# Performance work log

Hardware: AMD Instinct MI355X
Metric: run time of the kernel (lower is better)

## Reference

```python
import jax, jax.numpy as jnp
import numpy as np

D_MODEL = 512
NUM_HEADS = 8
HEAD_DIM = D_MODEL // NUM_HEADS  # 64


def setup_inputs() -> dict:
    key = jax.random.key(0)
    k_x, k_wqkv, k_bqkv, k_wout, k_bout = jax.random.split(key, 5)
    B, L = 30, 2048
    s_in = 1.0 / np.sqrt(D_MODEL)
    return {
        "x": jax.random.normal(k_x, (B, L, D_MODEL), dtype=jnp.float32),
        "w_qkv": jax.random.uniform(k_wqkv, (3 * D_MODEL, D_MODEL), minval=-s_in, maxval=s_in, dtype=jnp.float32),
        "b_qkv": jax.random.uniform(k_bqkv, (3 * D_MODEL,), minval=-s_in, maxval=s_in, dtype=jnp.float32),
        "w_out": jax.random.uniform(k_wout, (D_MODEL, D_MODEL), minval=-s_in, maxval=s_in, dtype=jnp.float32),
        "b_out": jax.random.uniform(k_bout, (D_MODEL,), minval=-s_in, maxval=s_in, dtype=jnp.float32),
    }


def reference(x, w_qkv, b_qkv, w_out, b_out):
    B, L, _ = x.shape
    # QKV projection: (B, L, 3*d_model)
    qkv = jnp.einsum("bld,ed->ble", x, w_qkv) + b_qkv
    # NOTE: source discards the permute, so layout stays (B, L, H, 3*head_dim)
    qkv = qkv.reshape(B, L, NUM_HEADS, 3 * HEAD_DIM)
    q, k, v = jnp.split(qkv, 3, axis=-1)  # each (B, L, H, head_dim)
    # Attention contracts head_dim -> (B, L, H, H): attention OVER HEADS, faithful to bug
    scores = jnp.einsum("blhd,blgd->blhg", q, k) / np.sqrt(HEAD_DIM)
    # mask=False in source adds 0 -> no-op
    attn = jax.nn.softmax(scores, axis=-1)
    val = jnp.einsum("blhg,blgd->blhd", attn, v).reshape(B, L, D_MODEL)
    out = jnp.einsum("bld,ed->ble", val, w_out) + b_out
    return out
```

## Files before the change

### kernel.cpp

```cpp
#include <hip/hip_runtime.h>
#include <hip/hip_bf16.h>
#include <stdint.h>

typedef short    s16x8  __attribute__((ext_vector_type(8)));
typedef __bf16   bf16x8 __attribute__((ext_vector_type(8)));
typedef float    f32x4  __attribute__((ext_vector_type(4)));

__device__ __forceinline__ unsigned short f2bf(float f) {
    union { float f; unsigned u; } v; v.f = f;
    unsigned r = v.u + 0x7FFFu + ((v.u >> 16) & 1u);
    return (unsigned short)(r >> 16);
}
__device__ __forceinline__ float bf2f(unsigned short s) {
    union { unsigned u; float f; } v; v.u = ((unsigned)s) << 16;
    return v.f;
}

__device__ __forceinline__ void gload16(const void* g, void* l) {
    __builtin_amdgcn_global_load_lds(
        (const __attribute__((address_space(1))) void*)(uintptr_t)g,
        (__attribute__((address_space(3))) void*)(uintptr_t)l,
        16, 0, 0);
}

__global__ __launch_bounds__(256) void cvt_bf16(const float* __restrict__ in,
                                                unsigned short* __restrict__ out,
                                                int n4) {
    int i = blockIdx.x * blockDim.x + threadIdx.x;
    int stride = gridDim.x * blockDim.x;
    for (; i < n4; i += stride) {
        const float4 v = *(const float4*)(in + (size_t)i * 4);
        ushort4 o;
        o.x = f2bf(v.x); o.y = f2bf(v.y); o.z = f2bf(v.z); o.w = f2bf(v.w);
        *(ushort4*)(out + (size_t)i * 4) = o;
    }
}

template<bool OUT_BF16>
__global__ __launch_bounds__(256) void gemm_bt(
        const unsigned short* __restrict__ A,
        const unsigned short* __restrict__ B,
        const float* __restrict__ bias,
        void* __restrict__ Cvoid,
        int M, int N, int K) {
    constexpr int BM = 128, BN = 128, BK = 32;
    __shared__ unsigned short As[BM * BK];
    __shared__ unsigned short Bs[BN * BK];
    const int tid  = threadIdx.x;
    const int lane = tid & 63;
    const int wv   = tid >> 6;
    const int ntn  = N / BN;
    const int bm   = (int)blockIdx.x / ntn;
    const int bn   = (int)blockIdx.x % ntn;
    const int wr   = (wv >> 1) * 64;
    const int wc   = (wv & 1) * 64;
    const int lr   = lane & 15;
    const int lk   = (lane >> 4) * 8;

    f32x4 acc[4][4] = {};

    for (int k0 = 0; k0 < K; k0 += BK) {
        #pragma unroll
        for (int i = 0; i < 2; ++i) {
            int f   = i * 4096 + tid * 16;
            int row = f >> 6;
            int col = (f & 63) >> 1;
            gload16(A + (size_t)(bm * BM + row) * K + k0 + col, (char*)As + f);
            gload16(B + (size_t)(bn * BN + row) * K + k0 + col, (char*)Bs + f);
        }
        __syncthreads();

        bf16x8 af[4], bfr[4];
        #pragma unroll
        for (int m = 0; m < 4; ++m)
            af[m] = *(const bf16x8*)(As + (wr + m * 16 + lr) * BK + lk);
        #pragma unroll
        for (int n = 0; n < 4; ++n)
            bfr[n] = *(const bf16x8*)(Bs + (wc + n * 16 + lr) * BK + lk);
        #pragma unroll
        for (int m = 0; m < 4; ++m)
            #pragma unroll
            for (int n = 0; n < 4; ++n)
                acc[m][n] = __builtin_amdgcn_mfma_f32_16x16x32_bf16(
                    af[m], bfr[n], acc[m][n], 0, 0, 0);
        __syncthreads();
    }

    const int r0 = bm * BM + wr + (lane >> 4) * 4;
    const int c0 = bn * BN + wc + lr;
    #pragma unroll
    for (int n = 0; n < 4; ++n) {
        const int gc = c0 + n * 16;
        const float bv = bias[gc];
        #pragma unroll
        for (int m = 0; m < 4; ++m) {
            #pragma unroll
            for (int j = 0; j < 4; ++j) {
                const int gr = r0 + m * 16 + j;
                const float v = acc[m][n][j] + bv;
                if constexpr (OUT_BF16)
                    ((unsigned short*)Cvoid)[(size_t)gr * N + gc] = f2bf(v);
                else
                    ((float*)Cvoid)[(size_t)gr * N + gc] = v;
            }
        }
    }
}

__global__ __launch_bounds__(256) void attn_heads(
        const unsigned short* __restrict__ qkv,
        unsigned short* __restrict__ val,
        int M) {
    const int t    = blockIdx.x * 4 + (threadIdx.x >> 6);
    const int lane = threadIdx.x & 63;
    const int h    = lane >> 3;
    const int c    = lane & 7;
    const unsigned short* base = qkv + (size_t)t * 1536;

    s16x8 q8 = *(const s16x8*)(base + h * 192 + c * 8);
    float qf[8];
    #pragma unroll
    for (int j = 0; j < 8; ++j) qf[j] = bf2f((unsigned short)q8[j]);

    float s[8];
    #pragma unroll
    for (int g = 0; g < 8; ++g) {
        s16x8 k8 = *(const s16x8*)(base + g * 192 + 64 + c * 8);
        float p = 0.f;
        #pragma unroll
        for (int j = 0; j < 8; ++j) p += qf[j] * bf2f((unsigned short)k8[j]);
        s[g] = p;
    }
    #pragma unroll
    for (int mask = 1; mask <= 4; mask <<= 1)
        #pragma unroll
        for (int g = 0; g < 8; ++g)
            s[g] += __shfl_xor(s[g], mask, 64);

    float mx = -1e30f;
    #pragma unroll
    for (int g = 0; g < 8; ++g) { s[g] *= 0.125f; mx = fmaxf(mx, s[g]); }
    float sum = 0.f;
    #pragma unroll
    for (int g = 0; g < 8; ++g) { s[g] = __expf(s[g] - mx); sum += s[g]; }
    const float inv = 1.f / sum;

    float acc[8] = {0.f,0.f,0.f,0.f,0.f,0.f,0.f,0.f};
    #pragma unroll
    for (int g = 0; g < 8; ++g) {
        s16x8 v8 = *(const s16x8*)(base + g * 192 + 128 + c * 8);
        const float ag = s[g] * inv;
        #pragma unroll
        for (int j = 0; j < 8; ++j) acc[j] += ag * bf2f((unsigned short)v8[j]);
    }
    s16x8 ov;
    #pragma unroll
    for (int j = 0; j < 8; ++j) ov[j] = (short)f2bf(acc[j]);
    *(s16x8*)(val + (size_t)t * 512 + h * 64 + c * 8) = ov;
}

extern "C" void kernel_launch(void* const* d_in, const int* in_sizes, int n_in,
                              void* d_out, int out_size, void* d_ws, size_t ws_size,
                              hipStream_t stream) {
    const float* x     = (const float*)d_in[0];
    const float* w_qkv = (const float*)d_in[1];
    const float* b_qkv = (const float*)d_in[2];
    const float* w_out = (const float*)d_in[3];
    const float* b_out = (const float*)d_in[4];
    float* out = (float*)d_out;

    const int DM = 512;
    const int M  = in_sizes[0] / DM;

    unsigned short* xb    = (unsigned short*)d_ws;
    unsigned short* wqkvb = xb + (size_t)M * DM;
    unsigned short* woutb = wqkvb + (size_t)3 * DM * DM;
    unsigned short* qkvb  = woutb + (size_t)DM * DM;
    unsigned short* valb  = xb;

    cvt_bf16<<<2048, 256, 0, stream>>>(x, xb, M * DM / 4);
    cvt_bf16<<<96,   256, 0, stream>>>(w_qkv, wqkvb, 3 * DM * DM / 4);
    cvt_bf16<<<32,   256, 0, stream>>>(w_out, woutb, DM * DM / 4);

    gemm_bt<true><<<dim3((M / 128) * (3 * DM / 128)), 256, 0, stream>>>(
        xb, wqkvb, b_qkv, qkvb, M, 3 * DM, DM);

    attn_heads<<<M / 4, 256, 0, stream>>>(qkvb, valb, M);

    gemm_bt<false><<<dim3((M / 128) * (DM / 128)), 256, 0, stream>>>(
        valb, woutb, b_out, out, M, DM, DM);
}
```

Measured before the change: 316.7 us.

## Replace GEMM with 256x256 double-buffered, swizzled-LDS, 8-wave kernel

Both projection GEMMs move to a 256x256 tile kernel with 512 threads, double-buffered LDS fed by direct global-to-LDS loads, an XOR swizzle against bank conflicts, and block-index remapping across XCDs. The K loop is fully unrolled at compile time, and MFMA phases are split with barriers and s_setprio so loads overlap compute. This targets memory stalls and sync overhead in the old single-buffer 128x128 kernel. It needs more LDS and registers per block and yields fewer blocks (M/256*6 = 1440 and 480), so occupancy and tail effects may change.

```diff
diff --git a/kernel.cpp b/kernel.cpp
--- a/kernel.cpp
+++ b/kernel.cpp
@@ -36,64 +36,102 @@
     }
 }
 
-template<bool OUT_BF16>
-__global__ __launch_bounds__(256) void gemm_bt(
+template<int K, bool OUT_BF16>
+__global__ __launch_bounds__(512, 2) void gemm256(
         const unsigned short* __restrict__ A,
         const unsigned short* __restrict__ B,
         const float* __restrict__ bias,
         void* __restrict__ Cvoid,
-        int M, int N, int K) {
-    constexpr int BM = 128, BN = 128, BK = 32;
-    __shared__ unsigned short As[BM * BK];
-    __shared__ unsigned short Bs[BN * BK];
+        int M, int N, int ntn) {
+    constexpr int BM = 256, BN = 256, BK = 32, NT = K / BK;
+    __shared__ unsigned short As[2][BM * BK];
+    __shared__ unsigned short Bs[2][BN * BK];
     const int tid  = threadIdx.x;
     const int lane = tid & 63;
     const int wv   = tid >> 6;
-    const int ntn  = N / BN;
-    const int bm   = (int)blockIdx.x / ntn;
-    const int bn   = (int)blockIdx.x % ntn;
-    const int wr   = (wv >> 1) * 64;
-    const int wc   = (wv & 1) * 64;
-    const int lr   = lane & 15;
-    const int lk   = (lane >> 4) * 8;
-
-    f32x4 acc[4][4] = {};
-
-    for (int k0 = 0; k0 < K; k0 += BK) {
-        #pragma unroll
-        for (int i = 0; i < 2; ++i) {
-            int f   = i * 4096 + tid * 16;
-            int row = f >> 6;
-            int col = (f & 63) >> 1;
-            gload16(A + (size_t)(bm * BM + row) * K + k0 + col, (char*)As + f);
-            gload16(B + (size_t)(bn * BN + row) * K + k0 + col, (char*)Bs + f);
+    const int nwg = (int)gridDim.x;
+    const int wg  = ((int)blockIdx.x & 7) * (nwg >> 3) + ((int)blockIdx.x >> 3);
+    const int bm  = wg / ntn;
+    const int bn  = wg % ntn;
+    const int wr  = (wv >> 2) * 128;
+    const int wc  = (wv & 3) * 64;
+    const int lr  = lane & 15;
+    const int ls  = lane >> 4;
+
+    const unsigned short* Ag = A + (size_t)bm * BM * K;
+    const unsigned short* Bg = B + (size_t)bn * BN * K;
+
+    auto stage = [&](const unsigned short* G, unsigned short* lds) {
+        #pragma unroll
+        for (int p = 0; p < 2; ++p) {
+            const int c     = p * 512 + tid;
+            const int row   = c >> 2;
+            const int slot  = c & 3;
+            const int gslot = slot ^ ((row >> 1) & 3);
+            gload16(G + (size_t)row * K + gslot * 8, (char*)lds + c * 16);
         }
-        __syncthreads();
-
-        bf16x8 af[4], bfr[4];
-        #pragma unroll
-        for (int m = 0; m < 4; ++m)
-            af[m] = *(const bf16x8*)(As + (wr + m * 16 + lr) * BK + lk);
-        #pragma unroll
-        for (int n = 0; n < 4; ++n)
-            bfr[n] = *(const bf16x8*)(Bs + (wc + n * 16 + lr) * BK + lk);
+    };
+    auto frag = [&](const unsigned short* lds, int row) -> bf16x8 {
+        const int slot = ls ^ ((row >> 1) & 3);
+        return *(const bf16x8*)((const char*)lds + row * (BK * 2) + slot * 16);
+    };
+
+    f32x4 acc[8][4] = {};
+
+    stage(Ag, As[0]);
+    stage(Bg, Bs[0]);
+
+    #pragma unroll
+    for (int t = 0; t < NT; ++t) {
+        const int cur = t & 1;
+        if (t + 1 < NT) {
+            stage(Ag + (t + 1) * BK, As[cur ^ 1]);
+            stage(Bg + (t + 1) * BK, Bs[cur ^ 1]);
+            asm volatile("s_waitcnt vmcnt(4)" ::: "memory");
+        } else {
+            asm volatile("s_waitcnt vmcnt(0)" ::: "memory");
+        }
+        __builtin_amdgcn_s_barrier();
+
+        bf16x8 a0[4], b0[4];
+        #pragma unroll
+        for (int m = 0; m < 4; ++m) a0[m] = frag(As[cur], wr + m * 16 + lr);
+        #pragma unroll
+        for (int n = 0; n < 4; ++n) b0[n] = frag(Bs[cur], wc + n * 16 + lr);
+        __builtin_amdgcn_s_barrier();
+        __builtin_amdgcn_s_setprio(1);
         #pragma unroll
         for (int m = 0; m < 4; ++m)
             #pragma unroll
             for (int n = 0; n < 4; ++n)
                 acc[m][n] = __builtin_amdgcn_mfma_f32_16x16x32_bf16(
-                    af[m], bfr[n], acc[m][n], 0, 0, 0);
-        __syncthreads();
-    }
-
-    const int r0 = bm * BM + wr + (lane >> 4) * 4;
+                    a0[m], b0[n], acc[m][n], 0, 0, 0);
+        __builtin_amdgcn_s_setprio(0);
+        __builtin_amdgcn_s_barrier();
+
+        bf16x8 a1[4];
+        #pragma unroll
+        for (int m = 0; m < 4; ++m) a1[m] = frag(As[cur], wr + 64 + m * 16 + lr);
+        __builtin_amdgcn_s_barrier();
+        __builtin_amdgcn_s_setprio(1);
+        #pragma unroll
+        for (int m = 0; m < 4; ++m)
+            #pragma unroll
+            for (int n = 0; n < 4; ++n)
+                acc[4 + m][n] = __builtin_amdgcn_mfma_f32_16x16x32_bf16(
+                    a1[m], b0[n], acc[4 + m][n], 0, 0, 0);
+        __builtin_amdgcn_s_setprio(0);
+        __builtin_amdgcn_s_barrier();
+    }
+
+    const int r0 = bm * BM + wr + ls * 4;
     const int c0 = bn * BN + wc + lr;
     #pragma unroll
     for (int n = 0; n < 4; ++n) {
         const int gc = c0 + n * 16;
         const float bv = bias[gc];
         #pragma unroll
-        for (int m = 0; m < 4; ++m) {
+        for (int m = 0; m < 8; ++m) {
             #pragma unroll
             for (int j = 0; j < 4; ++j) {
                 const int gr = r0 + m * 16 + j;
@@ -182,11 +220,11 @@
     cvt_bf16<<<96,   256, 0, stream>>>(w_qkv, wqkvb, 3 * DM * DM / 4);
     cvt_bf16<<<32,   256, 0, stream>>>(w_out, woutb, DM * DM / 4);
 
-    gemm_bt<true><<<dim3((M / 128) * (3 * DM / 128)), 256, 0, stream>>>(
-        xb, wqkvb, b_qkv, qkvb, M, 3 * DM, DM);
+    gemm256<512, true><<<dim3((M / 256) * (3 * DM / 256)), 512, 0, stream>>>(
+        xb, wqkvb, b_qkv, qkvb, M, 3 * DM, 3 * DM / 256);
 
     attn_heads<<<M / 4, 256, 0, stream>>>(qkvb, valb, M);
 
-    gemm_bt<false><<<dim3((M / 128) * (DM / 128)), 256, 0, stream>>>(
-        valb, woutb, b_out, out, M, DM, DM);
-}
+    gemm256<512, false><<<dim3((M / 256) * (DM / 256)), 512, 0, stream>>>(
+        valb, woutb, b_out, out, M, DM, DM / 256);
+}
```

After: 319.6 us. Within noise of the previous version (+0.9%).
